# Kernel optimization log

Measured on AMD Instinct MI355X. Metric: run time of the kernel, lower is better.

Reference implementation:

```python
import math
import jax, jax.numpy as jnp
import numpy as np

HEAD_DIM = 2
ROPE_PERIOD = 19.0
OMEGA = 2.0 * math.pi / ROPE_PERIOD
PEAK_EPS = 0.3
TARGET_LOGIT_GAP = math.log(10.0)
ATTN_AMPLITUDE = TARGET_LOGIT_GAP / (math.cos(OMEGA * PEAK_EPS) - math.cos(OMEGA * (1.0 - PEAK_EPS)))
QK_NORM_SCALE = math.sqrt(ATTN_AMPLITUDE / math.sqrt(2.0))
SCALE = HEAD_DIM ** (-0.5) * QK_NORM_SCALE ** 2
INTERMEDIATE_SIZE = 2
EMBED_CONST = 1000.0
B, L = 4, 4096


def _rms(x, eps=1e-6):
    return x * jax.lax.rsqrt(jnp.mean(x * x, axis=-1, keepdims=True) + eps)


def _rope(x):
    # x: (B, 1, L, 2)
    seq_len = x.shape[2]
    theta = jnp.arange(seq_len, dtype=x.dtype) * jnp.asarray(OMEGA, x.dtype)
    cos_t = jnp.cos(theta)[None, None, :, None]
    sin_t = jnp.sin(theta)[None, None, :, None]
    x0, x1 = x[..., 0:1], x[..., 1:2]
    return jnp.concatenate([x0 * cos_t - x1 * sin_t, x0 * sin_t + x1 * cos_t], axis=-1)


def setup_inputs() -> dict:
    key = jax.random.key(0)
    k1, k2, k3, k4, k5 = jax.random.split(key, 5)
    x = jax.random.normal(k1, (B, L, 2), dtype=jnp.float32)
    # causal additive mask (1, 1, L, L)
    causal = jnp.tril(jnp.ones((L, L), dtype=bool))
    mask = jnp.where(causal, 0.0, -1e9).astype(jnp.float32)[None, None]
    q_weight = jax.random.normal(k2, (1,), dtype=jnp.float32) * 0.1
    v_weight = jax.random.normal(k3, (1,), dtype=jnp.float32) * 0.1
    gate_weight = jax.random.normal(k4, (2,), dtype=jnp.float32) * 0.1
    carry_weight = jax.random.normal(k5, (1,), dtype=jnp.float32) * 0.1
    return {"x": x, "mask": mask, "q_weight": q_weight, "v_weight": v_weight,
            "gate_weight": gate_weight, "carry_weight": carry_weight}


def reference(x, mask, q_weight, v_weight, gate_weight, carry_weight):
    # ---- attention branch ----
    xn = _rms(x)                                    # (B, L, 2)
    phi = q_weight[0]
    q = jnp.stack([xn[..., 0] * jnp.cos(phi), xn[..., 0] * -jnp.sin(phi)], axis=-1)
    k = jnp.stack([xn[..., 0], jnp.zeros_like(xn[..., 0])], axis=-1)
    v = jnp.stack([xn[..., 1] * v_weight[0], jnp.zeros_like(xn[..., 0])], axis=-1)
    q, k, v = q[:, None], k[:, None], v[:, None]    # (B, 1, L, 2)
    q = _rope(_rms(q))
    k = _rope(_rms(k))
    attn = jnp.einsum('bhqd,bhkd->bhqk', q, k) * jnp.asarray(SCALE, x.dtype)
    attn = jax.nn.softmax(attn + mask, axis=-1)
    out = jnp.einsum('bhqk,bhkd->bhqd', attn, v)    # (B, 1, L, 2)
    o0 = out[:, 0, :, 0]                            # (B, L)
    attn_out = jnp.stack([jnp.zeros_like(o0), o0], axis=-1)  # OProj channel swap
    h = x + attn_out
    # ---- gated MLP branch ----
    hn = _rms(h)
    a, c = gate_weight[0], gate_weight[1]
    g0 = hn[..., 0] * a + hn[..., 1] * c
    g1 = hn[..., 0] * (a - c / EMBED_CONST) + hn[..., 1] * c
    base = hn[..., 0]
    mix0 = jax.nn.silu(g0) * base
    mix1 = jax.nn.silu(g1) * base
    y1 = carry_weight[0] * (mix1 - mix0)
    mlp_out = jnp.stack([jnp.zeros_like(y1), y1], axis=-1)
    return h + mlp_out
```

## Files before the change

kernel.cpp:

```cpp
#include <hip/hip_runtime.h>
#include <math.h>

#define SEQ_L 4096
#define LDS_PAD 260

__device__ __forceinline__ float wave_sum_dpp(float x) {
    int t;
    t = __builtin_amdgcn_update_dpp(0, __float_as_int(x), 0x111, 0xf, 0xf, true); x += __int_as_float(t);
    t = __builtin_amdgcn_update_dpp(0, __float_as_int(x), 0x112, 0xf, 0xf, true); x += __int_as_float(t);
    t = __builtin_amdgcn_update_dpp(0, __float_as_int(x), 0x114, 0xf, 0xf, true); x += __int_as_float(t);
    t = __builtin_amdgcn_update_dpp(0, __float_as_int(x), 0x118, 0xf, 0xf, true); x += __int_as_float(t);
    t = __builtin_amdgcn_update_dpp(0, __float_as_int(x), 0x142, 0xa, 0xf, true); x += __int_as_float(t);
    t = __builtin_amdgcn_update_dpp(0, __float_as_int(x), 0x143, 0xc, 0xf, true); x += __int_as_float(t);
    return x;
}

#define FEXP2(dst, t2s, u, Bs) { \
    float bf_ = fmaf((t2s), (u), (Bs)); \
    bf_ = fmaxf(bf_, 8388608.0f); \
    dst = __int_as_float((int)bf_); }

__device__ __forceinline__ void do_group_half(
    int b0, int lane, int h,
    const float* As, const float* Ws, float* Pout,
    float scaleL2, float cphi, float sphi,
    float cd, float sd, float cd2, float sd2,
    float ck1, float sk1, float ck2, float sk2, float ck3, float sk3)
{
    const float SQRT2 = 1.4142135623730951f;
    const float EXPSC = 8388608.0f;
    const float EXPB  = 126.956945f;
    const int i0 = b0, i1 = b0 + 19, i2 = b0 + 38, i3 = b0 + 57;
    const int c1 = i1 < SEQ_L ? i1 : SEQ_L - 1;
    const int c2 = i2 < SEQ_L ? i2 : SEQ_L - 1;
    const int c3 = i3 < SEQ_L ? i3 : SEQ_L - 1;

    const float t20 = scaleL2 * As[i0], t21 = scaleL2 * As[c1];
    const float t22 = scaleL2 * As[c2], t23 = scaleL2 * As[c3];
    const float t2s0 = t20 * EXPSC, t2s1 = t21 * EXPSC;
    const float t2s2 = t22 * EXPSC, t2s3 = t23 * EXPSC;
    const float Bs0 = (EXPB - fabsf(t20) * SQRT2) * EXPSC;
    const float Bs1 = (EXPB - fabsf(t21) * SQRT2) * EXPSC;
    const float Bs2 = (EXPB - fabsf(t22) * SQRT2) * EXPSC;
    const float Bs3 = (EXPB - fabsf(t23) * SQRT2) * EXPSC;

    unsigned r = (unsigned)(b0 - (lane << 2) + 266) % 19u;
    float rev = (float)r * (1.0f / 19.0f);
    float crv = __builtin_amdgcn_cosf(rev);
    float srv = __builtin_amdgcn_sinf(rev);
    float C = fmaf(srv, sphi, crv * cphi);
    float S = fmaf(crv, -sphi, srv * cphi);
    if (h) {
        float Cn = fmaf(S, sd, C * cd);
        float Sn = fmaf(S, cd, -(C * sd));
        C = Cn; S = Sn;
    }

    float sa0=0.f, sa1=0.f, sa2=0.f, sa3=0.f;
    float oa0=0.f, oa1=0.f, oa2=0.f, oa3=0.f;
    int jb = (lane << 2) + (h << 8);
    const int ncom = (b0 + 1) >> 8;
    const int T    = (c3 >> 8) + 1;

#define EL4S(u, pw) { \
    float e0_, e1_, e2_, e3_; \
    FEXP2(e0_, t2s0, (u), Bs0) \
    FEXP2(e1_, t2s1, (u), Bs1) \
    FEXP2(e2_, t2s2, (u), Bs2) \
    FEXP2(e3_, t2s3, (u), Bs3) \
    sa0 += e0_; oa0 = fmaf(e0_, (pw), oa0); \
    sa1 += e1_; oa1 = fmaf(e1_, (pw), oa1); \
    sa2 += e2_; oa2 = fmaf(e2_, (pw), oa2); \
    sa3 += e3_; oa3 = fmaf(e3_, (pw), oa3); }
#define ELM4S(u, pw, jj) { \
    float e0_, e1_, e2_, e3_; \
    FEXP2(e0_, t2s0, (u), Bs0) \
    FEXP2(e1_, t2s1, (u), Bs1) \
    FEXP2(e2_, t2s2, (u), Bs2) \
    FEXP2(e3_, t2s3, (u), Bs3) \
    e0_ = ((jj) <= i0) ? e0_ : 0.f; \
    e1_ = ((jj) <= i1) ? e1_ : 0.f; \
    e2_ = ((jj) <= i2) ? e2_ : 0.f; \
    e3_ = ((jj) <= i3) ? e3_ : 0.f; \
    sa0 += e0_; oa0 = fmaf(e0_, (pw), oa0); \
    sa1 += e1_; oa1 = fmaf(e1_, (pw), oa1); \
    sa2 += e2_; oa2 = fmaf(e2_, (pw), oa2); \
    sa3 += e3_; oa3 = fmaf(e3_, (pw), oa3); }
#define ROT2() { \
    float Cn_ = fmaf(S, sd2, C * cd2); \
    float Sn_ = fmaf(S, cd2, -(C * sd2)); \
    C = Cn_; S = Sn_; }

    int t = h;
    for (; t < ncom; t += 2) {
        float4 av = *(const float4*)&As[jb];
        float4 wv = *(const float4*)&Ws[jb];
        float C1 = fmaf(S, sk1, C * ck1);
        float C2 = fmaf(S, sk2, C * ck2);
        float C3 = fmaf(S, sk3, C * ck3);
        float u0 = av.x * C,  u1 = av.y * C1;
        float u2 = av.z * C2, u3 = av.w * C3;
        EL4S(u0, wv.x) EL4S(u1, wv.y) EL4S(u2, wv.z) EL4S(u3, wv.w)
        ROT2();
        jb += 512;
    }
    for (; t < T; t += 2) {
        float4 av = *(const float4*)&As[jb];
        float4 wv = *(const float4*)&Ws[jb];
        float C1 = fmaf(S, sk1, C * ck1);
        float C2 = fmaf(S, sk2, C * ck2);
        float C3 = fmaf(S, sk3, C * ck3);
        float u0 = av.x * C,  u1 = av.y * C1;
        float u2 = av.z * C2, u3 = av.w * C3;
        ELM4S(u0, wv.x, jb)     ELM4S(u1, wv.y, jb + 1)
        ELM4S(u2, wv.z, jb + 2) ELM4S(u3, wv.w, jb + 3)
        ROT2();
        jb += 512;
    }
#undef EL4S
#undef ELM4S
#undef ROT2

    float S0 = wave_sum_dpp(sa0), O0 = wave_sum_dpp(oa0);
    float S1 = wave_sum_dpp(sa1), O1 = wave_sum_dpp(oa1);
    float S2 = wave_sum_dpp(sa2), O2 = wave_sum_dpp(oa2);
    float S3 = wave_sum_dpp(sa3), O3 = wave_sum_dpp(oa3);

    if (lane == 63) {
        Pout[0] = S0; Pout[1] = O0;
        Pout[2] = S1; Pout[3] = O1;
        Pout[4] = S2; Pout[5] = O2;
        Pout[6] = S3; Pout[7] = O3;
    }
}

__global__ __launch_bounds__(256, 4) void attn_rows_kernel(
    const float* __restrict__ x,
    const float* __restrict__ q_weight,
    const float* __restrict__ v_weight,
    const float* __restrict__ gate_weight,
    const float* __restrict__ carry_weight,
    float* __restrict__ out,
    float scaleL2,
    float cd, float sd,
    float cd2, float sd2,
    float ck1, float sk1, float ck2, float sk2, float ck3, float sk3)
{
    __shared__ float As[SEQ_L + LDS_PAD];
    __shared__ float Ws[SEQ_L + LDS_PAD];
    __shared__ float P[2][2][16];

    const int tid  = threadIdx.x;
    const int lane = tid & 63;
    const int wave = tid >> 6;
    const int pl   = wave >> 1;
    const int h    = wave & 1;
    const int bat  = blockIdx.x / 257;
    const int bb   = blockIdx.x % 257;

    const float phi = q_weight[0];
    const float vw  = v_weight[0];
    const float2* x2 = (const float2*)x + (size_t)bat * SEQ_L;
    float2* outp = (float2*)out + (size_t)bat * SEQ_L;

    const float INV2PI = 0.15915494309189535f;
    const float rphi = phi * INV2PI;
    const float cphi = __builtin_amdgcn_cosf(rphi);
    const float sphi = __builtin_amdgcn_sinf(rphi);

    const float4* x4 = (const float4*)x2;
    #pragma unroll
    for (int it = 0; it < 8; ++it) {
        int idx = tid + (it << 8);
        float4 v = x4[idx];
        int e0 = idx << 1, e1 = e0 + 1;
        float inv0 = __builtin_amdgcn_rsqf(fmaf(v.x, v.x*0.5f, fmaf(v.y, v.y*0.5f, 1e-6f)));
        float xn0a = v.x * inv0;
        As[e0] = xn0a * __builtin_amdgcn_rsqf(fmaf(xn0a, xn0a*0.5f, 1e-6f));
        Ws[e0] = v.y * inv0 * vw;
        float inv1 = __builtin_amdgcn_rsqf(fmaf(v.z, v.z*0.5f, fmaf(v.w, v.w*0.5f, 1e-6f)));
        float xn0b = v.z * inv1;
        As[e1] = xn0b * __builtin_amdgcn_rsqf(fmaf(xn0b, xn0b*0.5f, 1e-6f));
        Ws[e1] = v.w * inv1 * vw;
    }
    __syncthreads();

    const int p = bb * 2 + pl;
    const bool active = (p < 513);
    int b0A = 0, b0B = 0;
    if (active) {
        const int m = p / 19;
        const int c = p - 19 * m;
        b0A = 76 * m + c;
        b0B = 4046 - b0A;
        do_group_half(b0A, lane, h, As, Ws, &P[pl][h][0],
                      scaleL2, cphi, sphi, cd, sd, cd2, sd2,
                      ck1, sk1, ck2, sk2, ck3, sk3);
        do_group_half(b0B, lane, h, As, Ws, &P[pl][h][8],
                      scaleL2, cphi, sphi, cd, sd, cd2, sd2,
                      ck1, sk1, ck2, sk2, ck3, sk3);
    }
    __syncthreads();

    if (active && h == 0 && lane < 8) {
        const float ga = gate_weight[0];
        const float gc = gate_weight[1];
        const float cw = carry_weight[0];
        const float LOG2E = 1.4426950408889634f;

        const int rsub = lane & 3;
        const int i = (lane < 4) ? (b0A + 19 * rsub) : (b0B + 19 * rsub);
        const int k = lane * 2;
        if (i < SEQ_L) {
            float s = P[pl][0][k]     + P[pl][1][k];
            float o = P[pl][0][k + 1] + P[pl][1][k + 1];
            float o0 = o * __builtin_amdgcn_rcpf(s);
            float2 xv = x2[i];
            float h0 = xv.x, h1 = xv.y + o0;
            float inv = __builtin_amdgcn_rsqf(
                           fmaf(h0, h0*0.5f, fmaf(h1, h1*0.5f, 1e-6f)));
            float hn0 = h0 * inv, hn1 = h1 * inv;
            float g0 = hn0 * ga + hn1 * gc;
            float g1 = hn0 * (ga - gc * 1e-3f) + hn1 * gc;
            float sg0 = __builtin_amdgcn_rcpf(1.f + __builtin_amdgcn_exp2f(-g0 * LOG2E));
            float sg1 = __builtin_amdgcn_rcpf(1.f + __builtin_amdgcn_exp2f(-g1 * LOG2E));
            float y1 = cw * (g1 * sg1 - g0 * sg0) * hn0;
            outp[i] = make_float2(h0, h1 + y1);
        }
    }
}

extern "C" void kernel_launch(void* const* d_in, const int* in_sizes, int n_in,
                              void* d_out, int out_size, void* d_ws, size_t ws_size,
                              hipStream_t stream)
{
    const float* x  = (const float*)d_in[0];
    const float* qw = (const float*)d_in[2];
    const float* vw = (const float*)d_in[3];
    const float* gw = (const float*)d_in[4];
    const float* cw = (const float*)d_in[5];
    float* out = (float*)d_out;

    const double omega = 2.0 * M_PI / 19.0;
    const double amp   = log(10.0) / (cos(omega * 0.3) - cos(omega * 0.7));
    const double qkns2 = amp / sqrt(2.0);
    const double scale = pow(2.0, -0.5) * qkns2;
    const double L2E   = 1.4426950408889634074;
    const double d1    = 256.0 * omega;
    const double d2    = 512.0 * omega;

    attn_rows_kernel<<<dim3(4 * 257), dim3(256), 0, stream>>>(
        x, qw, vw, gw, cw, out,
        (float)(scale * L2E),
        (float)cos(d1),          (float)sin(d1),
        (float)cos(d2),          (float)sin(d2),
        (float)cos(omega),       (float)sin(omega),
        (float)cos(2.0 * omega), (float)sin(2.0 * omega),
        (float)cos(3.0 * omega), (float)sin(3.0 * omega));
}
```

Baseline: 17.55 us.

## Vectorize exp-accumulate loop with packed float2 math and prefetch next LDS tile

Rewrites the inner softmax-accumulation loop to use two-wide float vectors so the compiler can emit packed FMA and max instructions (v_pk_fma_f32 on CDNA). It replaces the per-element causal select with an additive large-negative mask folded into the FMA, and software-pipelines the LDS loads by fetching the next tile one iteration ahead. The LDS padding is enlarged and zero-filled so the one-ahead prefetch past the end stays in bounds. It risks more register pressure and extra packing moves if the compiler does not form packed ops, and the clamp against zero instead of the old exponent floor changes underflow behaviour.

Result: no change. 17.78 us (+1.3%).

```diff
diff --git a/kernel.cpp b/kernel.cpp
--- a/kernel.cpp
+++ b/kernel.cpp
@@ -2,7 +2,10 @@
 #include <math.h>
 
 #define SEQ_L 4096
-#define LDS_PAD 260
+#define LDS_PAD 524
+
+typedef float v2f __attribute__((ext_vector_type(2)));
+__device__ __forceinline__ v2f mk2(float a, float b) { v2f r; r.x = a; r.y = b; return r; }
 
 __device__ __forceinline__ float wave_sum_dpp(float x) {
     int t;
@@ -14,11 +17,6 @@
     t = __builtin_amdgcn_update_dpp(0, __float_as_int(x), 0x143, 0xc, 0xf, true); x += __int_as_float(t);
     return x;
 }
-
-#define FEXP2(dst, t2s, u, Bs) { \
-    float bf_ = fmaf((t2s), (u), (Bs)); \
-    bf_ = fmaxf(bf_, 8388608.0f); \
-    dst = __int_as_float((int)bf_); }
 
 __device__ __forceinline__ void do_group_half(
     int b0, int lane, int h,
@@ -37,12 +35,17 @@
 
     const float t20 = scaleL2 * As[i0], t21 = scaleL2 * As[c1];
     const float t22 = scaleL2 * As[c2], t23 = scaleL2 * As[c3];
-    const float t2s0 = t20 * EXPSC, t2s1 = t21 * EXPSC;
-    const float t2s2 = t22 * EXPSC, t2s3 = t23 * EXPSC;
     const float Bs0 = (EXPB - fabsf(t20) * SQRT2) * EXPSC;
     const float Bs1 = (EXPB - fabsf(t21) * SQRT2) * EXPSC;
     const float Bs2 = (EXPB - fabsf(t22) * SQRT2) * EXPSC;
     const float Bs3 = (EXPB - fabsf(t23) * SQRT2) * EXPSC;
+    const v2f T0 = mk2(t20 * EXPSC, t20 * EXPSC);
+    const v2f T1 = mk2(t21 * EXPSC, t21 * EXPSC);
+    const v2f T2 = mk2(t22 * EXPSC, t22 * EXPSC);
+    const v2f T3 = mk2(t23 * EXPSC, t23 * EXPSC);
+    const v2f B0 = mk2(Bs0, Bs0), B1 = mk2(Bs1, Bs1);
+    const v2f B2 = mk2(Bs2, Bs2), B3 = mk2(Bs3, Bs3);
+    const v2f z2 = mk2(0.f, 0.f);
 
     unsigned r = (unsigned)(b0 - (lane << 2) + 266) % 19u;
     float rev = (float)r * (1.0f / 19.0f);
@@ -56,75 +59,89 @@
         C = Cn; S = Sn;
     }
 
-    float sa0=0.f, sa1=0.f, sa2=0.f, sa3=0.f;
-    float oa0=0.f, oa1=0.f, oa2=0.f, oa3=0.f;
+    v2f sa0 = z2, sa1 = z2, sa2 = z2, sa3 = z2;
+    v2f oa0 = z2, oa1 = z2, oa2 = z2, oa3 = z2;
     int jb = (lane << 2) + (h << 8);
     const int ncom = (b0 + 1) >> 8;
     const int T    = (c3 >> 8) + 1;
 
-#define EL4S(u, pw) { \
-    float e0_, e1_, e2_, e3_; \
-    FEXP2(e0_, t2s0, (u), Bs0) \
-    FEXP2(e1_, t2s1, (u), Bs1) \
-    FEXP2(e2_, t2s2, (u), Bs2) \
-    FEXP2(e3_, t2s3, (u), Bs3) \
-    sa0 += e0_; oa0 = fmaf(e0_, (pw), oa0); \
-    sa1 += e1_; oa1 = fmaf(e1_, (pw), oa1); \
-    sa2 += e2_; oa2 = fmaf(e2_, (pw), oa2); \
-    sa3 += e3_; oa3 = fmaf(e3_, (pw), oa3); }
-#define ELM4S(u, pw, jj) { \
-    float e0_, e1_, e2_, e3_; \
-    FEXP2(e0_, t2s0, (u), Bs0) \
-    FEXP2(e1_, t2s1, (u), Bs1) \
-    FEXP2(e2_, t2s2, (u), Bs2) \
-    FEXP2(e3_, t2s3, (u), Bs3) \
-    e0_ = ((jj) <= i0) ? e0_ : 0.f; \
-    e1_ = ((jj) <= i1) ? e1_ : 0.f; \
-    e2_ = ((jj) <= i2) ? e2_ : 0.f; \
-    e3_ = ((jj) <= i3) ? e3_ : 0.f; \
-    sa0 += e0_; oa0 = fmaf(e0_, (pw), oa0); \
-    sa1 += e1_; oa1 = fmaf(e1_, (pw), oa1); \
-    sa2 += e2_; oa2 = fmaf(e2_, (pw), oa2); \
-    sa3 += e3_; oa3 = fmaf(e3_, (pw), oa3); }
+#define ROWP(Tm, Bm, sam, oam) { \
+    v2f a01_ = __builtin_elementwise_fma(u01, Tm, Bm); \
+    v2f a23_ = __builtin_elementwise_fma(u23, Tm, Bm); \
+    a01_ = __builtin_elementwise_max(a01_, z2); \
+    a23_ = __builtin_elementwise_max(a23_, z2); \
+    v2f e01_ = mk2(__int_as_float((int)a01_.x), __int_as_float((int)a01_.y)); \
+    v2f e23_ = mk2(__int_as_float((int)a23_.x), __int_as_float((int)a23_.y)); \
+    sam += e01_ + e23_; \
+    oam = __builtin_elementwise_fma(e01_, w01, oam); \
+    oam = __builtin_elementwise_fma(e23_, w23, oam); }
+
+#define ROWPM(Tm, Bm, sam, oam, mb01, mb23) { \
+    v2f a01_ = __builtin_elementwise_fma(u01, Tm, Bm) + (mb01); \
+    v2f a23_ = __builtin_elementwise_fma(u23, Tm, Bm) + (mb23); \
+    a01_ = __builtin_elementwise_max(a01_, z2); \
+    a23_ = __builtin_elementwise_max(a23_, z2); \
+    v2f e01_ = mk2(__int_as_float((int)a01_.x), __int_as_float((int)a01_.y)); \
+    v2f e23_ = mk2(__int_as_float((int)a23_.x), __int_as_float((int)a23_.y)); \
+    sam += e01_ + e23_; \
+    oam = __builtin_elementwise_fma(e01_, w01, oam); \
+    oam = __builtin_elementwise_fma(e23_, w23, oam); }
+
 #define ROT2() { \
     float Cn_ = fmaf(S, sd2, C * cd2); \
     float Sn_ = fmaf(S, cd2, -(C * sd2)); \
     C = Cn_; S = Sn_; }
 
+    float4 av = *(const float4*)&As[jb];
+    float4 wv = *(const float4*)&Ws[jb];
     int t = h;
     for (; t < ncom; t += 2) {
-        float4 av = *(const float4*)&As[jb];
-        float4 wv = *(const float4*)&Ws[jb];
+        float4 avn = *(const float4*)&As[jb + 512];
+        float4 wvn = *(const float4*)&Ws[jb + 512];
         float C1 = fmaf(S, sk1, C * ck1);
         float C2 = fmaf(S, sk2, C * ck2);
         float C3 = fmaf(S, sk3, C * ck3);
-        float u0 = av.x * C,  u1 = av.y * C1;
-        float u2 = av.z * C2, u3 = av.w * C3;
-        EL4S(u0, wv.x) EL4S(u1, wv.y) EL4S(u2, wv.z) EL4S(u3, wv.w)
+        v2f u01 = mk2(av.x, av.y) * mk2(C,  C1);
+        v2f u23 = mk2(av.z, av.w) * mk2(C2, C3);
+        v2f w01 = mk2(wv.x, wv.y);
+        v2f w23 = mk2(wv.z, wv.w);
+        ROWP(T0, B0, sa0, oa0) ROWP(T1, B1, sa1, oa1)
+        ROWP(T2, B2, sa2, oa2) ROWP(T3, B3, sa3, oa3)
         ROT2();
-        jb += 512;
+        av = avn; wv = wvn; jb += 512;
     }
     for (; t < T; t += 2) {
-        float4 av = *(const float4*)&As[jb];
-        float4 wv = *(const float4*)&Ws[jb];
+        float4 avn = *(const float4*)&As[jb + 512];
+        float4 wvn = *(const float4*)&Ws[jb + 512];
         float C1 = fmaf(S, sk1, C * ck1);
         float C2 = fmaf(S, sk2, C * ck2);
         float C3 = fmaf(S, sk3, C * ck3);
-        float u0 = av.x * C,  u1 = av.y * C1;
-        float u2 = av.z * C2, u3 = av.w * C3;
-        ELM4S(u0, wv.x, jb)     ELM4S(u1, wv.y, jb + 1)
-        ELM4S(u2, wv.z, jb + 2) ELM4S(u3, wv.w, jb + 3)
+        v2f u01 = mk2(av.x, av.y) * mk2(C,  C1);
+        v2f u23 = mk2(av.z, av.w) * mk2(C2, C3);
+        v2f w01 = mk2(wv.x, wv.y);
+        v2f w23 = mk2(wv.z, wv.w);
+        const float MB = -3.0e9f;
+        v2f m0a = mk2(jb + 0 <= i0 ? 0.f : MB, jb + 1 <= i0 ? 0.f : MB);
+        v2f m0b = mk2(jb + 2 <= i0 ? 0.f : MB, jb + 3 <= i0 ? 0.f : MB);
+        v2f m1a = mk2(jb + 0 <= i1 ? 0.f : MB, jb + 1 <= i1 ? 0.f : MB);
+        v2f m1b = mk2(jb + 2 <= i1 ? 0.f : MB, jb + 3 <= i1 ? 0.f : MB);
+        v2f m2a = mk2(jb + 0 <= i2 ? 0.f : MB, jb + 1 <= i2 ? 0.f : MB);
+        v2f m2b = mk2(jb + 2 <= i2 ? 0.f : MB, jb + 3 <= i2 ? 0.f : MB);
+        v2f m3a = mk2(jb + 0 <= i3 ? 0.f : MB, jb + 1 <= i3 ? 0.f : MB);
+        v2f m3b = mk2(jb + 2 <= i3 ? 0.f : MB, jb + 3 <= i3 ? 0.f : MB);
+        ROWPM(T0, B0, sa0, oa0, m0a, m0b) ROWPM(T1, B1, sa1, oa1, m1a, m1b)
+        ROWPM(T2, B2, sa2, oa2, m2a, m2b) ROWPM(T3, B3, sa3, oa3, m3a, m3b)
         ROT2();
-        jb += 512;
-    }
-#undef EL4S
-#undef ELM4S
+        av = avn; wv = wvn; jb += 512;
+    }
+#undef ROWP
+#undef ROWPM
 #undef ROT2
 
-    float S0 = wave_sum_dpp(sa0), O0 = wave_sum_dpp(oa0);
-    float S1 = wave_sum_dpp(sa1), O1 = wave_sum_dpp(oa1);
-    float S2 = wave_sum_dpp(sa2), O2 = wave_sum_dpp(oa2);
-    float S3 = wave_sum_dpp(sa3), O3 = wave_sum_dpp(oa3);
+    float S0 = wave_sum_dpp(sa0.x + sa0.y), O0 = wave_sum_dpp(oa0.x + oa0.y);
+    float S1 = wave_sum_dpp(sa1.x + sa1.y), O1 = wave_sum_dpp(oa1.x + oa1.y);
+    float S2 = wave_sum_dpp(sa2.x + sa2.y), O2 = wave_sum_dpp(oa2.x + oa2.y);
+    float S3 = wave_sum_dpp(sa3.x + sa3.y), O3 = wave_sum_dpp(oa3.x + oa3.y);
 
     if (lane == 63) {
         Pout[0] = S0; Pout[1] = O0;
@@ -182,6 +199,10 @@
         float xn0b = v.z * inv1;
         As[e1] = xn0b * __builtin_amdgcn_rsqf(fmaf(xn0b, xn0b*0.5f, 1e-6f));
         Ws[e1] = v.w * inv1 * vw;
+    }
+    for (int z = tid; z < LDS_PAD; z += 256) {
+        As[SEQ_L + z] = 0.f;
+        Ws[SEQ_L + z] = 0.f;
     }
     __syncthreads();
 
```
